# Performance work log

Hardware: AMD Instinct MI355X
Metric: run time of the kernel (lower is better)

The kernel has to match this reference:

```python
import jax, jax.numpy as jnp
import numpy as np

N = 100000   # nodes
E = 1600000  # edges
D = 64       # in_channels
H = 64       # hidden_channels
G = 1000     # number of graphs (100 nodes each)


def _xavier(key, fan_in, fan_out):
    a = np.sqrt(6.0 / (fan_in + fan_out)).astype(np.float32)
    return jax.random.uniform(key, (fan_in, fan_out), jnp.float32, -a, a)


def setup_inputs() -> dict:
    key = jax.random.key(0)
    ks = jax.random.split(key, 6)
    x = jax.random.normal(ks[0], (N, D), jnp.float32)
    edge_index = jax.random.randint(ks[1], (2, E), 0, N, dtype=jnp.int32)
    edge_weight = jax.random.uniform(ks[2], (E,), jnp.float32)
    # every graph id 0..G-1 occurs exactly N//G times (sorted)
    batch = (jnp.arange(N, dtype=jnp.int32) // (N // G)).astype(jnp.int32)
    W1 = _xavier(ks[3], D, H); b1 = jnp.zeros((H,), jnp.float32)
    W2 = _xavier(ks[4], H, H); b2 = jnp.zeros((H,), jnp.float32)
    W3 = _xavier(ks[5], H, 1); b3 = jnp.zeros((1,), jnp.float32)
    return dict(x=x, edge_index=edge_index, edge_weight=edge_weight, batch=batch,
                W1=W1, b1=b1, W2=W2, b2=b2, W3=W3, b3=b3)


def reference(x, edge_index, edge_weight, batch, W1, b1, W2, b2, W3, b3):
    src, dst = edge_index[0], edge_index[1]
    # nodes per graph (torch.bincount(batch)) and broadcast back to nodes
    counts = jax.ops.segment_sum(jnp.ones((N,), jnp.float32), batch, num_segments=G)
    cpn = counts[batch]  # [N]

    def mpnn_layer(h, W, b):
        # gather x_j, scale by edge weight, scatter-add to target nodes
        m = h[src] * edge_weight[:, None]              # [E, C]
        agg = jax.ops.segment_sum(m, dst, num_segments=N)  # [N, C]
        out = agg / cpn[:, None]                       # per-node normalize
        return out @ W + b

    h = jax.nn.sigmoid(mpnn_layer(x, W1, b1))
    h = jax.nn.sigmoid(mpnn_layer(h, W2, b2))
    h = mpnn_layer(h, W3, b3)                          # [N, 1]
    # global mean pool over each graph
    pooled = jax.ops.segment_sum(h, batch, num_segments=G) / counts[:, None]
    return pooled  # [G, 1]
```

## Files before the change

### kernel.cpp

```cpp
#include <hip/hip_runtime.h>
#include <hip/hip_fp16.h>
#include <math.h>

#define NN 100000
#define EE 1600000
#define GG 1000
#define NPG 100
#define NBUK 391
#define BCAP 4608
#define EPB 8192
#define NBINBLK ((EE + EPB - 1) / EPB)
#define GEMM1BLK ((NN + 127) / 128)
#define GEMM2BLK ((NN + 63) / 64)

typedef __attribute__((ext_vector_type(8))) short short8v;
typedef __attribute__((ext_vector_type(4))) float float4v;

__device__ __forceinline__ unsigned char f32_to_fp8(float a) {
    return (unsigned char)(__builtin_amdgcn_cvt_pk_fp8_f32(a, a, 0, false) & 0xFF);
}
__device__ __forceinline__ float fp8_to_f32(unsigned b) {
    return __builtin_amdgcn_cvt_f32_fp8((int)b, 0);
}
__device__ __forceinline__ unsigned short f32_to_bf16(float f) {
    unsigned u = __float_as_uint(f);
    unsigned r = u + 0x7FFFu + ((u >> 16) & 1u);
    return (unsigned short)(r >> 16);
}

#if __has_builtin(__builtin_amdgcn_cvt_pk_f32_fp8)
typedef float floatx2 __attribute__((ext_vector_type(2)));
#define HAVE_PK_CVT 1
#else
#define HAVE_PK_CVT 0
#endif

__device__ __forceinline__ void unpack4(unsigned dw, float* f) {
#if HAVE_PK_CVT
    floatx2 lo = __builtin_amdgcn_cvt_pk_f32_fp8(dw, false);
    floatx2 hi = __builtin_amdgcn_cvt_pk_f32_fp8(dw, true);
    f[0] = lo.x; f[1] = lo.y; f[2] = hi.x; f[3] = hi.y;
#else
    f[0] = fp8_to_f32(dw & 0xFF);
    f[1] = fp8_to_f32((dw >> 8) & 0xFF);
    f[2] = fp8_to_f32((dw >> 16) & 0xFF);
    f[3] = fp8_to_f32((dw >> 24) & 0xFF);
#endif
}

__device__ __forceinline__ float4v mfma16(short8v a, short8v b, float4v c) {
    return __builtin_amdgcn_mfma_f32_16x16x32_bf16(a, b, c, 0, 0, 0);
}
__device__ __forceinline__ short8v fp8x8_to_bf16frag(uint2 q) {
    float f[8];
    unpack4(q.x, f);
    unpack4(q.y, f + 4);
    short8v s;
#pragma unroll
    for (int j = 0; j < 8; j++) s[j] = (short)f32_to_bf16(f[j]);
    return s;
}
__device__ __forceinline__ short8v f32x8_to_bf16frag(float4 a, float4 b) {
    short8v s;
    s[0] = (short)f32_to_bf16(a.x); s[1] = (short)f32_to_bf16(a.y);
    s[2] = (short)f32_to_bf16(a.z); s[3] = (short)f32_to_bf16(a.w);
    s[4] = (short)f32_to_bf16(b.x); s[5] = (short)f32_to_bf16(b.y);
    s[6] = (short)f32_to_bf16(b.z); s[7] = (short)f32_to_bf16(b.w);
    return s;
}
template<int NT>
__device__ __forceinline__ void stageW(const float* __restrict__ W,
                                       unsigned short* Wt, int tid) {
    for (int i = tid; i < 4096; i += NT) {
        int k = i >> 6, c = i & 63;
        Wt[(c << 6) | (((k >> 3) ^ (c & 7)) << 3) | (k & 7)] = f32_to_bf16(W[i]);
    }
}
__device__ __forceinline__ short8v ldB(const unsigned short* Wt, int col, int g) {
    return *(const short8v*)&Wt[(col << 6) | ((g ^ (col & 7)) << 3)];
}
__device__ __forceinline__ void mfma_tile_store(short8v a_lo, short8v a_hi,
                                                const unsigned short* Wt,
                                                int row0, int lane,
                                                unsigned char* __restrict__ out, int n) {
    int rl = lane & 15, kg = lane >> 4;
#pragma unroll
    for (int ct = 0; ct < 4; ct++) {
        int col = ct * 16 + rl;
        short8v blo = ldB(Wt, col, kg);
        short8v bhi = ldB(Wt, col, 4 + kg);
        float4v acc = {0.f, 0.f, 0.f, 0.f};
        acc = mfma16(a_lo, blo, acc);
        acc = mfma16(a_hi, bhi, acc);
        int dr = (lane >> 4) * 4;
#pragma unroll
        for (int r = 0; r < 4; r++) {
            int R = row0 + dr + r;
            if (R < n) out[(size_t)R * 64 + col] = f32_to_fp8(acc[r]);
        }
    }
}

__global__ __launch_bounds__(512)
void k_binbound(const int* __restrict__ src, const int* __restrict__ dst,
                const float* __restrict__ ew, int* __restrict__ bukcnt,
                uint2* __restrict__ ep1, int* __restrict__ rowptr, int E) {
    __shared__ int hist[NBUK];
    __shared__ int gbase[NBUK];
    int tid = threadIdx.x;
    if (blockIdx.x == 0 && tid == 0) rowptr[NN] = EE;
    for (int i = tid; i < NBUK; i += 512) hist[i] = 0;
    __syncthreads();
    int base = blockIdx.x * EPB;
    int b[16], rank[16];
    unsigned x[16], w[16];
#pragma unroll
    for (int u = 0; u < 16; u++) {
        int e = base + u * 512 + tid;
        if (e < E) {
            int d = dst[e];
            b[u] = d >> 8;
            x[u] = ((unsigned)(d & 255) << 24) | (unsigned)src[e];
            w[u] = __float_as_uint(ew[e]);
            rank[u] = atomicAdd(&hist[b[u]], 1);
        } else b[u] = -1;
    }
    __syncthreads();
    for (int i = tid; i < NBUK; i += 512) {
        int h = hist[i];
        gbase[i] = h ? atomicAdd(&bukcnt[i], h) : 0;
    }
    __syncthreads();
#pragma unroll
    for (int u = 0; u < 16; u++) {
        if (b[u] >= 0) ep1[(size_t)b[u] * BCAP + gbase[b[u]] + rank[u]] = make_uint2(x[u], w[u]);
    }
}

__global__ __launch_bounds__(512)
void k_bin2gemm1(const uint2* __restrict__ ep1, const int* __restrict__ bukcnt,
                 unsigned* __restrict__ ep2, int* __restrict__ rowptr,
                 const float* __restrict__ x, const float* __restrict__ W1,
                 unsigned char* __restrict__ t, int n) {
    __shared__ __align__(16) unsigned char smem[41984];
    int tid = threadIdx.x;
    int bk = blockIdx.x;
    if (bk < NBUK) {
        uint2* stage = (uint2*)smem;
        int* h   = (int*)(smem + 36864);
        int* s   = h + 256;
        int* cur = s + 256;
        int* sc  = cur + 256;
        int v = (tid < NBUK) ? bukcnt[tid] : 0;
        sc[tid] = v;
        __syncthreads();
        for (int off = 1; off < 512; off <<= 1) {
            int tv = (tid >= off) ? sc[tid - off] : 0;
            __syncthreads();
            sc[tid] += tv;
            __syncthreads();
        }
        int cnt = bukcnt[bk];
        int base = sc[bk] - cnt;
        if (tid < 256) h[tid] = 0;
        __syncthreads();
        size_t ebase = (size_t)bk * BCAP;
        for (int e = tid; e < cnt; e += 512) {
            uint2 r = ep1[ebase + e];
            stage[e] = r;
            atomicAdd(&h[r.x >> 24], 1);
        }
        __syncthreads();
        if (tid < 256) s[tid] = h[tid];
        __syncthreads();
        for (int off = 1; off < 256; off <<= 1) {
            int tv = 0;
            if (tid < 256 && tid >= off) tv = s[tid - off];
            __syncthreads();
            if (tid < 256) s[tid] += tv;
            __syncthreads();
        }
        if (tid < 256) {
            int pfx = base + s[tid] - h[tid];
            int node = bk * 256 + tid;
            if (node < n) rowptr[node] = pfx;
            cur[tid] = pfx;
        }
        __syncthreads();
        for (int e = tid; e < cnt; e += 512) {
            uint2 r = stage[e];
            int pos = atomicAdd(&cur[r.x >> 24], 1);
            unsigned wq = (unsigned)fminf(__uint_as_float(r.y) * 32768.f + 0.5f, 32767.f);
            ep2[pos] = (wq << 17) | (r.x & 0x1FFFFu);
        }
    } else {
        unsigned short* Wt = (unsigned short*)smem;
        stageW<512>(W1, Wt, tid);
        __syncthreads();
        int w = tid >> 6, lane = tid & 63;
        int row0 = (bk - NBUK) * 128 + w * 16;
        int rl = lane & 15, kg = lane >> 4;
        int rsrc = row0 + rl;
        if (rsrc > n - 1) rsrc = n - 1;
        const float* ar = x + (size_t)rsrc * 64 + kg * 8;
        float4 f0 = *(const float4*)ar;
        float4 f1 = *(const float4*)(ar + 4);
        float4 f2 = *(const float4*)(ar + 32);
        float4 f3 = *(const float4*)(ar + 36);
        short8v a_lo = f32x8_to_bf16frag(f0, f1);
        short8v a_hi = f32x8_to_bf16frag(f2, f3);
        mfma_tile_store(a_lo, a_hi, Wt, row0, lane, t, n);
    }
}

__global__ __launch_bounds__(256)
void k_gemm64_mfma(const unsigned char* __restrict__ inp, const float* __restrict__ W,
                   unsigned char* __restrict__ out, int n) {
    __shared__ __align__(16) unsigned short Wt[64 * 64];
    int tid = threadIdx.x;
    stageW<256>(W, Wt, tid);
    __syncthreads();
    int w = tid >> 6, lane = tid & 63;
    int row0 = blockIdx.x * 64 + w * 16;
    int rl = lane & 15, kg = lane >> 4;
    int rsrc = row0 + rl;
    if (rsrc > n - 1) rsrc = n - 1;
    const unsigned char* ar = inp + (size_t)rsrc * 64 + kg * 8;
    uint2 qlo = *(const uint2*)ar;
    uint2 qhi = *(const uint2*)(ar + 32);
    short8v a_lo = fp8x8_to_bf16frag(qlo);
    short8v a_hi = fp8x8_to_bf16frag(qhi);
    mfma_tile_store(a_lo, a_hi, Wt, row0, lane, out, n);
}

template<int MODE>
__global__ __launch_bounds__(256)
void k_gather64(const unsigned char* __restrict__ t, const int* __restrict__ rowptr,
                const unsigned* __restrict__ ep, void* __restrict__ outp,
                const float* __restrict__ bv, const float* __restrict__ W3,
                int nq) {
    int wid = (blockIdx.x * blockDim.x + threadIdx.x) >> 6;
    int lane = threadIdx.x & 63;
    wid = __builtin_amdgcn_readfirstlane(wid);
    if (wid >= nq) return;
    int n0 = wid * 4;
    int q = lane >> 4;
    unsigned sl4 = (unsigned)(lane & 15) * 4u;

    int rp[5];
#pragma unroll
    for (int i = 0; i < 5; i++) rp[i] = rowptr[n0 + i];

    unsigned wl[4];
#pragma unroll
    for (int i = 0; i < 4; i++) {
        int e = rp[i] + lane;
        wl[i] = (e < rp[i + 1]) ? ep[e] : 0u;
    }

    unsigned vA[4][4];
#pragma unroll
    for (int i = 0; i < 4; i++) {
#pragma unroll
        for (int g = 0; g < 4; g++) {
            unsigned wq = __shfl(wl[i], g * 4 + q, 64);
            vA[i][g] = *(const unsigned*)(t + ((wq & 0x1FFFFu) * 64u + sl4));
        }
    }
    unsigned vB[4][4];
#pragma unroll
    for (int i = 0; i < 4; i++) {
        if (rp[i + 1] - rp[i] > 16) {
#pragma unroll
            for (int g = 0; g < 4; g++) {
                unsigned wq = __shfl(wl[i], 16 + g * 4 + q, 64);
                vB[i][g] = *(const unsigned*)(t + ((wq & 0x1FFFFu) * 64u + sl4));
            }
        }
    }

    const float Cn = 0x1p-15f / (float)NPG;
    float4 bb = ((const float4*)bv)[lane & 15];
    float4 w4 = (MODE == 1) ? ((const float4*)W3)[lane & 15] : make_float4(0, 0, 0, 0);

#pragma unroll
    for (int i = 0; i < 4; i++) {
        float ax = 0.f, ay = 0.f, az = 0.f, aw = 0.f;
#pragma unroll
        for (int g = 0; g < 4; g++) {
            unsigned wq = __shfl(wl[i], g * 4 + q, 64);
            float wt = (float)(wq >> 17);
            float f[4];
            unpack4(vA[i][g], f);
            ax = fmaf(wt, f[0], ax); ay = fmaf(wt, f[1], ay);
            az = fmaf(wt, f[2], az); aw = fmaf(wt, f[3], aw);
        }
        if (rp[i + 1] - rp[i] > 16) {
#pragma unroll
            for (int g = 0; g < 4; g++) {
                unsigned wq = __shfl(wl[i], 16 + g * 4 + q, 64);
                float wt = (float)(wq >> 17);
                float f[4];
                unpack4(vB[i][g], f);
                ax = fmaf(wt, f[0], ax); ay = fmaf(wt, f[1], ay);
                az = fmaf(wt, f[2], az); aw = fmaf(wt, f[3], aw);
            }
        }
        for (int e = rp[i] + 32 + q; e < rp[i + 1]; e += 4) {
            unsigned wq = ep[e];
            float wt = (float)(wq >> 17);
            float f[4];
            unpack4(*(const unsigned*)(t + ((wq & 0x1FFFFu) * 64u + sl4)), f);
            ax = fmaf(wt, f[0], ax); ay = fmaf(wt, f[1], ay);
            az = fmaf(wt, f[2], az); aw = fmaf(wt, f[3], aw);
        }
        ax += __shfl_xor(ax, 16, 64); ax += __shfl_xor(ax, 32, 64);
        ay += __shfl_xor(ay, 16, 64); ay += __shfl_xor(ay, 32, 64);
        az += __shfl_xor(az, 16, 64); az += __shfl_xor(az, 32, 64);
        aw += __shfl_xor(aw, 16, 64); aw += __shfl_xor(aw, 32, 64);
        float v0 = ax * Cn + bb.x, v1 = ay * Cn + bb.y;
        float v2 = az * Cn + bb.z, v3 = aw * Cn + bb.w;
        v0 = 1.f / (1.f + __expf(-v0));
        v1 = 1.f / (1.f + __expf(-v1));
        v2 = 1.f / (1.f + __expf(-v2));
        v3 = 1.f / (1.f + __expf(-v3));
        if (MODE == 0) {
            if (q == 0) {
                unsigned r = (unsigned)__builtin_amdgcn_cvt_pk_fp8_f32(v0, v1, 0, false);
                r = (unsigned)__builtin_amdgcn_cvt_pk_fp8_f32(v2, v3, (int)r, true);
                ((unsigned*)outp)[(size_t)(n0 + i) * 16 + (lane & 15)] = r;
            }
        } else {
            float d = v0 * w4.x + v1 * w4.y + v2 * w4.z + v3 * w4.w;
            d += __shfl_xor(d, 1, 64);
            d += __shfl_xor(d, 2, 64);
            d += __shfl_xor(d, 4, 64);
            d += __shfl_xor(d, 8, 64);
            if (lane == 0) ((float*)outp)[n0 + i] = d;
        }
    }
}

__global__ __launch_bounds__(256)
void k_y3pool(const float* __restrict__ y, const int* __restrict__ rowptr,
              const unsigned* __restrict__ ep,
              const float* __restrict__ b3, float* __restrict__ out) {
    __shared__ float red[256];
    int g = blockIdx.x;
    int tid = threadIdx.x;
    int ebeg = rowptr[g * NPG], eend = rowptr[g * NPG + NPG];
    float acc = 0.f;
    for (int e = ebeg + tid; e < eend; e += 256) {
        unsigned r = ep[e];
        unsigned off = (r & 0x1FFFFu) * 4u;
        acc = fmaf((float)(r >> 17), *(const float*)((const char*)y + off), acc);
    }
    red[tid] = acc;
    __syncthreads();
    for (int off = 128; off > 0; off >>= 1) {
        if (tid < off) red[tid] += red[tid + off];
        __syncthreads();
    }
    if (tid == 0) {
        out[g] = red[0] * 0x1p-15f / ((float)NPG * (float)NPG) + b3[0];
    }
}

extern "C" void kernel_launch(void* const* d_in, const int* in_sizes, int n_in,
                              void* d_out, int out_size, void* d_ws, size_t ws_size,
                              hipStream_t stream) {
    const float* x     = (const float*)d_in[0];
    const int*   ei    = (const int*)d_in[1];
    const int*   src   = ei;
    const int*   dst   = ei + EE;
    const float* ew    = (const float*)d_in[2];
    const float* W1    = (const float*)d_in[4];
    const float* b1    = (const float*)d_in[5];
    const float* W2    = (const float*)d_in[6];
    const float* b2    = (const float*)d_in[7];
    const float* W3    = (const float*)d_in[8];
    const float* b3    = (const float*)d_in[9];
    float* out = (float*)d_out;

    unsigned char* t   = (unsigned char*)d_ws;
    unsigned char* t2  = t + (size_t)NN * 64;
    unsigned char* hh8 = t2 + (size_t)NN * 64;
    float* y      = (float*)(hh8 + (size_t)NN * 64);
    unsigned* ep2 = (unsigned*)(y + NN);
    int*   bukcnt = (int*)(ep2 + EE);
    int*   rowptr = bukcnt + NBUK + 1;
    uint2* ep1    = (uint2*)(rowptr + NN + 2);

    hipMemsetAsync(bukcnt, 0, NBUK * sizeof(int), stream);

    k_binbound<<<NBINBLK, 512, 0, stream>>>(src, dst, ew, bukcnt, ep1, rowptr, EE);

    k_bin2gemm1<<<NBUK + GEMM1BLK, 512, 0, stream>>>(ep1, bukcnt, ep2, rowptr, x, W1, t, NN);

    int nq = NN / 4;
    int gblk = (nq * 64 + 255) / 256;

    k_gather64<0><<<gblk, 256, 0, stream>>>(t, rowptr, ep2, hh8, b1, nullptr, nq);

    k_gemm64_mfma<<<GEMM2BLK, 256, 0, stream>>>(hh8, W2, t2, NN);

    k_gather64<1><<<gblk, 256, 0, stream>>>(t2, rowptr, ep2, y, b2, W3, nq);

    k_y3pool<<<GG, 256, 0, stream>>>(y, rowptr, ep2, b3, out);
}
```

Before: 204.8 us.

## Make gather kernel persistent with software-prefetch of next quad's edge lists

```diff
diff --git a/kernel.cpp b/kernel.cpp
--- a/kernel.cpp
+++ b/kernel.cpp
@@ -12,6 +12,7 @@
 #define NBINBLK ((EE + EPB - 1) / EPB)
 #define GEMM1BLK ((NN + 127) / 128)
 #define GEMM2BLK ((NN + 63) / 64)
+#define GATHBLK 1536
 
 typedef __attribute__((ext_vector_type(8))) short short8v;
 typedef __attribute__((ext_vector_type(4))) float float4v;
@@ -239,105 +240,128 @@
                 const unsigned* __restrict__ ep, void* __restrict__ outp,
                 const float* __restrict__ bv, const float* __restrict__ W3,
                 int nq) {
-    int wid = (blockIdx.x * blockDim.x + threadIdx.x) >> 6;
     int lane = threadIdx.x & 63;
-    wid = __builtin_amdgcn_readfirstlane(wid);
-    if (wid >= nq) return;
-    int n0 = wid * 4;
+    int wv = (blockIdx.x * blockDim.x + threadIdx.x) >> 6;
+    wv = __builtin_amdgcn_readfirstlane(wv);
+    int nwv = (GATHBLK * 256) >> 6;
     int q = lane >> 4;
     unsigned sl4 = (unsigned)(lane & 15) * 4u;
-
-    int rp[5];
-#pragma unroll
-    for (int i = 0; i < 5; i++) rp[i] = rowptr[n0 + i];
-
-    unsigned wl[4];
-#pragma unroll
-    for (int i = 0; i < 4; i++) {
-        int e = rp[i] + lane;
-        wl[i] = (e < rp[i + 1]) ? ep[e] : 0u;
-    }
-
-    unsigned vA[4][4];
-#pragma unroll
-    for (int i = 0; i < 4; i++) {
-#pragma unroll
-        for (int g = 0; g < 4; g++) {
-            unsigned wq = __shfl(wl[i], g * 4 + q, 64);
-            vA[i][g] = *(const unsigned*)(t + ((wq & 0x1FFFFu) * 64u + sl4));
-        }
-    }
-    unsigned vB[4][4];
-#pragma unroll
-    for (int i = 0; i < 4; i++) {
-        if (rp[i + 1] - rp[i] > 16) {
-#pragma unroll
-            for (int g = 0; g < 4; g++) {
-                unsigned wq = __shfl(wl[i], 16 + g * 4 + q, 64);
-                vB[i][g] = *(const unsigned*)(t + ((wq & 0x1FFFFu) * 64u + sl4));
-            }
-        }
-    }
-
     const float Cn = 0x1p-15f / (float)NPG;
     float4 bb = ((const float4*)bv)[lane & 15];
     float4 w4 = (MODE == 1) ? ((const float4*)W3)[lane & 15] : make_float4(0, 0, 0, 0);
 
+    int quad = wv;
+    if (quad >= nq) return;
+
+    int rpA[5];
+    unsigned wlA[4];
+#pragma unroll
+    for (int i = 0; i < 5; i++) rpA[i] = rowptr[quad * 4 + i];
 #pragma unroll
     for (int i = 0; i < 4; i++) {
-        float ax = 0.f, ay = 0.f, az = 0.f, aw = 0.f;
-#pragma unroll
-        for (int g = 0; g < 4; g++) {
-            unsigned wq = __shfl(wl[i], g * 4 + q, 64);
-            float wt = (float)(wq >> 17);
-            float f[4];
-            unpack4(vA[i][g], f);
-            ax = fmaf(wt, f[0], ax); ay = fmaf(wt, f[1], ay);
-            az = fmaf(wt, f[2], az); aw = fmaf(wt, f[3], aw);
-        }
-        if (rp[i + 1] - rp[i] > 16) {
+        int e = rpA[i] + lane;
+        wlA[i] = (e < rpA[i + 1]) ? ep[e] : 0u;
+    }
+
+    while (true) {
+        int nxt = quad + nwv;
+        bool hn = nxt < nq;
+        int rpB[5];
+        if (hn) {
+#pragma unroll
+            for (int i = 0; i < 5; i++) rpB[i] = rowptr[nxt * 4 + i];
+        }
+        unsigned vA[4][4];
+#pragma unroll
+        for (int i = 0; i < 4; i++) {
 #pragma unroll
             for (int g = 0; g < 4; g++) {
-                unsigned wq = __shfl(wl[i], 16 + g * 4 + q, 64);
+                unsigned wq = __shfl(wlA[i], g * 4 + q, 64);
+                vA[i][g] = *(const unsigned*)(t + ((wq & 0x1FFFFu) * 64u + sl4));
+            }
+        }
+        unsigned vB[4][4];
+#pragma unroll
+        for (int i = 0; i < 4; i++) {
+            if (rpA[i + 1] - rpA[i] > 16) {
+#pragma unroll
+                for (int g = 0; g < 4; g++) {
+                    unsigned wq = __shfl(wlA[i], 16 + g * 4 + q, 64);
+                    vB[i][g] = *(const unsigned*)(t + ((wq & 0x1FFFFu) * 64u + sl4));
+                }
+            }
+        }
+        unsigned wlB[4];
+        if (hn) {
+#pragma unroll
+            for (int i = 0; i < 4; i++) {
+                int e = rpB[i] + lane;
+                wlB[i] = (e < rpB[i + 1]) ? ep[e] : 0u;
+            }
+        }
+        int n0 = quad * 4;
+#pragma unroll
+        for (int i = 0; i < 4; i++) {
+            float ax = 0.f, ay = 0.f, az = 0.f, aw = 0.f;
+#pragma unroll
+            for (int g = 0; g < 4; g++) {
+                unsigned wq = __shfl(wlA[i], g * 4 + q, 64);
                 float wt = (float)(wq >> 17);
                 float f[4];
-                unpack4(vB[i][g], f);
+                unpack4(vA[i][g], f);
                 ax = fmaf(wt, f[0], ax); ay = fmaf(wt, f[1], ay);
                 az = fmaf(wt, f[2], az); aw = fmaf(wt, f[3], aw);
             }
-        }
-        for (int e = rp[i] + 32 + q; e < rp[i + 1]; e += 4) {
-            unsigned wq = ep[e];
-            float wt = (float)(wq >> 17);
-            float f[4];
-            unpack4(*(const unsigned*)(t + ((wq & 0x1FFFFu) * 64u + sl4)), f);
-            ax = fmaf(wt, f[0], ax); ay = fmaf(wt, f[1], ay);
-            az = fmaf(wt, f[2], az); aw = fmaf(wt, f[3], aw);
-        }
-        ax += __shfl_xor(ax, 16, 64); ax += __shfl_xor(ax, 32, 64);
-        ay += __shfl_xor(ay, 16, 64); ay += __shfl_xor(ay, 32, 64);
-        az += __shfl_xor(az, 16, 64); az += __shfl_xor(az, 32, 64);
-        aw += __shfl_xor(aw, 16, 64); aw += __shfl_xor(aw, 32, 64);
-        float v0 = ax * Cn + bb.x, v1 = ay * Cn + bb.y;
-        float v2 = az * Cn + bb.z, v3 = aw * Cn + bb.w;
-        v0 = 1.f / (1.f + __expf(-v0));
-        v1 = 1.f / (1.f + __expf(-v1));
-        v2 = 1.f / (1.f + __expf(-v2));
-        v3 = 1.f / (1.f + __expf(-v3));
-        if (MODE == 0) {
-            if (q == 0) {
-                unsigned r = (unsigned)__builtin_amdgcn_cvt_pk_fp8_f32(v0, v1, 0, false);
-                r = (unsigned)__builtin_amdgcn_cvt_pk_fp8_f32(v2, v3, (int)r, true);
-                ((unsigned*)outp)[(size_t)(n0 + i) * 16 + (lane & 15)] = r;
-            }
-        } else {
-            float d = v0 * w4.x + v1 * w4.y + v2 * w4.z + v3 * w4.w;
-            d += __shfl_xor(d, 1, 64);
-            d += __shfl_xor(d, 2, 64);
-            d += __shfl_xor(d, 4, 64);
-            d += __shfl_xor(d, 8, 64);
-            if (lane == 0) ((float*)outp)[n0 + i] = d;
-        }
+            if (rpA[i + 1] - rpA[i] > 16) {
+#pragma unroll
+                for (int g = 0; g < 4; g++) {
+                    unsigned wq = __shfl(wlA[i], 16 + g * 4 + q, 64);
+                    float wt = (float)(wq >> 17);
+                    float f[4];
+                    unpack4(vB[i][g], f);
+                    ax = fmaf(wt, f[0], ax); ay = fmaf(wt, f[1], ay);
+                    az = fmaf(wt, f[2], az); aw = fmaf(wt, f[3], aw);
+                }
+            }
+            for (int e = rpA[i] + 32 + q; e < rpA[i + 1]; e += 4) {
+                unsigned wq = ep[e];
+                float wt = (float)(wq >> 17);
+                float f[4];
+                unpack4(*(const unsigned*)(t + ((wq & 0x1FFFFu) * 64u + sl4)), f);
+                ax = fmaf(wt, f[0], ax); ay = fmaf(wt, f[1], ay);
+                az = fmaf(wt, f[2], az); aw = fmaf(wt, f[3], aw);
+            }
+            ax += __shfl_xor(ax, 16, 64); ax += __shfl_xor(ax, 32, 64);
+            ay += __shfl_xor(ay, 16, 64); ay += __shfl_xor(ay, 32, 64);
+            az += __shfl_xor(az, 16, 64); az += __shfl_xor(az, 32, 64);
+            aw += __shfl_xor(aw, 16, 64); aw += __shfl_xor(aw, 32, 64);
+            float v0 = ax * Cn + bb.x, v1 = ay * Cn + bb.y;
+            float v2 = az * Cn + bb.z, v3 = aw * Cn + bb.w;
+            v0 = 1.f / (1.f + __expf(-v0));
+            v1 = 1.f / (1.f + __expf(-v1));
+            v2 = 1.f / (1.f + __expf(-v2));
+            v3 = 1.f / (1.f + __expf(-v3));
+            if (MODE == 0) {
+                if (q == 0) {
+                    unsigned r = (unsigned)__builtin_amdgcn_cvt_pk_fp8_f32(v0, v1, 0, false);
+                    r = (unsigned)__builtin_amdgcn_cvt_pk_fp8_f32(v2, v3, (int)r, true);
+                    ((unsigned*)outp)[(size_t)(n0 + i) * 16 + (lane & 15)] = r;
+                }
+            } else {
+                float d = v0 * w4.x + v1 * w4.y + v2 * w4.z + v3 * w4.w;
+                d += __shfl_xor(d, 1, 64);
+                d += __shfl_xor(d, 2, 64);
+                d += __shfl_xor(d, 4, 64);
+                d += __shfl_xor(d, 8, 64);
+                if (lane == 0) ((float*)outp)[n0 + i] = d;
+            }
+        }
+        if (!hn) break;
+        quad = nxt;
+#pragma unroll
+        for (int i = 0; i < 5; i++) rpA[i] = rpB[i];
+#pragma unroll
+        for (int i = 0; i < 4; i++) wlA[i] = wlB[i];
     }
 }
 
@@ -398,13 +422,12 @@
     k_bin2gemm1<<<NBUK + GEMM1BLK, 512, 0, stream>>>(ep1, bukcnt, ep2, rowptr, x, W1, t, NN);
 
     int nq = NN / 4;
-    int gblk = (nq * 64 + 255) / 256;
-
-    k_gather64<0><<<gblk, 256, 0, stream>>>(t, rowptr, ep2, hh8, b1, nullptr, nq);
+
+    k_gather64<0><<<GATHBLK, 256, 0, stream>>>(t, rowptr, ep2, hh8, b1, nullptr, nq);
 
     k_gemm64_mfma<<<GEMM2BLK, 256, 0, stream>>>(hh8, W2, t2, NN);
 
-    k_gather64<1><<<gblk, 256, 0, stream>>>(t2, rowptr, ep2, y, b2, W3, nq);
+    k_gather64<1><<<GATHBLK, 256, 0, stream>>>(t2, rowptr, ep2, y, b2, W3, nq);
 
     k_y3pool<<<GG, 256, 0, stream>>>(y, rowptr, ep2, b3, out);
 }
```

After: 213.2 us. 1.04x slower.

## Fuse layer-2 GEMM into first gather kernel via shared-memory MFMA tile

Applied to the files above, without the earlier changes.

```diff
diff --git a/kernel.cpp b/kernel.cpp
--- a/kernel.cpp
+++ b/kernel.cpp
@@ -11,7 +11,6 @@
 #define EPB 8192
 #define NBINBLK ((EE + EPB - 1) / EPB)
 #define GEMM1BLK ((NN + 127) / 128)
-#define GEMM2BLK ((NN + 63) / 64)
 
 typedef __attribute__((ext_vector_type(8))) short short8v;
 typedef __attribute__((ext_vector_type(4))) float float4v;
@@ -50,15 +49,6 @@
 
 __device__ __forceinline__ float4v mfma16(short8v a, short8v b, float4v c) {
     return __builtin_amdgcn_mfma_f32_16x16x32_bf16(a, b, c, 0, 0, 0);
-}
-__device__ __forceinline__ short8v fp8x8_to_bf16frag(uint2 q) {
-    float f[8];
-    unpack4(q.x, f);
-    unpack4(q.y, f + 4);
-    short8v s;
-#pragma unroll
-    for (int j = 0; j < 8; j++) s[j] = (short)f32_to_bf16(f[j]);
-    return s;
 }
 __device__ __forceinline__ short8v f32x8_to_bf16frag(float4 a, float4 b) {
     short8v s;
@@ -213,34 +203,20 @@
     }
 }
 
-__global__ __launch_bounds__(256)
-void k_gemm64_mfma(const unsigned char* __restrict__ inp, const float* __restrict__ W,
-                   unsigned char* __restrict__ out, int n) {
-    __shared__ __align__(16) unsigned short Wt[64 * 64];
-    int tid = threadIdx.x;
-    stageW<256>(W, Wt, tid);
-    __syncthreads();
-    int w = tid >> 6, lane = tid & 63;
-    int row0 = blockIdx.x * 64 + w * 16;
-    int rl = lane & 15, kg = lane >> 4;
-    int rsrc = row0 + rl;
-    if (rsrc > n - 1) rsrc = n - 1;
-    const unsigned char* ar = inp + (size_t)rsrc * 64 + kg * 8;
-    uint2 qlo = *(const uint2*)ar;
-    uint2 qhi = *(const uint2*)(ar + 32);
-    short8v a_lo = fp8x8_to_bf16frag(qlo);
-    short8v a_hi = fp8x8_to_bf16frag(qhi);
-    mfma_tile_store(a_lo, a_hi, Wt, row0, lane, out, n);
-}
-
 template<int MODE>
 __global__ __launch_bounds__(256)
 void k_gather64(const unsigned char* __restrict__ t, const int* __restrict__ rowptr,
                 const unsigned* __restrict__ ep, void* __restrict__ outp,
                 const float* __restrict__ bv, const float* __restrict__ W3,
+                const float* __restrict__ W2, unsigned char* __restrict__ t2,
                 int nq) {
-    int wid = (blockIdx.x * blockDim.x + threadIdx.x) >> 6;
-    int lane = threadIdx.x & 63;
+    __shared__ __align__(16) unsigned short Wt[4096];
+    __shared__ __align__(16) unsigned short H1[1024];
+    int tid = threadIdx.x;
+    if (MODE == 0) stageW<256>(W2, Wt, tid);
+
+    int wid = (blockIdx.x * blockDim.x + tid) >> 6;
+    int lane = tid & 63;
     wid = __builtin_amdgcn_readfirstlane(wid);
     if (wid >= nq) return;
     int n0 = wid * 4;
@@ -326,9 +302,15 @@
         v3 = 1.f / (1.f + __expf(-v3));
         if (MODE == 0) {
             if (q == 0) {
-                unsigned r = (unsigned)__builtin_amdgcn_cvt_pk_fp8_f32(v0, v1, 0, false);
-                r = (unsigned)__builtin_amdgcn_cvt_pk_fp8_f32(v2, v3, (int)r, true);
-                ((unsigned*)outp)[(size_t)(n0 + i) * 16 + (lane & 15)] = r;
+                int s = lane & 15;
+                int row = (tid >> 6) * 4 + i;
+                unsigned g = (unsigned)(s >> 1);
+                unsigned off = ((unsigned)row << 6) | ((g ^ (unsigned)(row & 7)) << 3)
+                             | ((unsigned)(s & 1) << 2);
+                H1[off    ] = f32_to_bf16(v0);
+                H1[off + 1] = f32_to_bf16(v1);
+                H1[off + 2] = f32_to_bf16(v2);
+                H1[off + 3] = f32_to_bf16(v3);
             }
         } else {
             float d = v0 * w4.x + v1 * w4.y + v2 * w4.z + v3 * w4.w;
@@ -337,6 +319,28 @@
             d += __shfl_xor(d, 4, 64);
             d += __shfl_xor(d, 8, 64);
             if (lane == 0) ((float*)outp)[n0 + i] = d;
+        }
+    }
+
+    if (MODE == 0) {
+        __syncthreads();
+        int w = tid >> 6;
+        int rl = lane & 15, kg = lane >> 4;
+        short8v a_lo = *(const short8v*)&H1[((unsigned)rl << 6)
+                        | (((unsigned)kg ^ (unsigned)(rl & 7)) << 3)];
+        short8v a_hi = *(const short8v*)&H1[((unsigned)rl << 6)
+                        | ((((unsigned)kg + 4u) ^ (unsigned)(rl & 7)) << 3)];
+        int col = w * 16 + rl;
+        short8v blo = ldB(Wt, col, kg);
+        short8v bhi = ldB(Wt, col, 4 + kg);
+        float4v acc = {0.f, 0.f, 0.f, 0.f};
+        acc = mfma16(a_lo, blo, acc);
+        acc = mfma16(a_hi, bhi, acc);
+        int row0 = blockIdx.x * 16;
+        int dr = kg * 4;
+#pragma unroll
+        for (int r = 0; r < 4; r++) {
+            t2[(size_t)(row0 + dr + r) * 64 + col] = f32_to_fp8(acc[r]);
         }
     }
 }
@@ -384,8 +388,7 @@
 
     unsigned char* t   = (unsigned char*)d_ws;
     unsigned char* t2  = t + (size_t)NN * 64;
-    unsigned char* hh8 = t2 + (size_t)NN * 64;
-    float* y      = (float*)(hh8 + (size_t)NN * 64);
+    float* y      = (float*)(t2 + (size_t)NN * 64);
     unsigned* ep2 = (unsigned*)(y + NN);
     int*   bukcnt = (int*)(ep2 + EE);
     int*   rowptr = bukcnt + NBUK + 1;
@@ -398,13 +401,11 @@
     k_bin2gemm1<<<NBUK + GEMM1BLK, 512, 0, stream>>>(ep1, bukcnt, ep2, rowptr, x, W1, t, NN);
 
     int nq = NN / 4;
-    int gblk = (nq * 64 + 255) / 256;
-
-    k_gather64<0><<<gblk, 256, 0, stream>>>(t, rowptr, ep2, hh8, b1, nullptr, nq);
-
-    k_gemm64_mfma<<<GEMM2BLK, 256, 0, stream>>>(hh8, W2, t2, NN);
-
-    k_gather64<1><<<gblk, 256, 0, stream>>>(t2, rowptr, ep2, y, b2, W3, nq);
+    int gblk = (nq * 64) / 256;
+
+    k_gather64<0><<<gblk, 256, 0, stream>>>(t, rowptr, ep2, nullptr, b1, nullptr, W2, t2, nq);
+
+    k_gather64<1><<<gblk, 256, 0, stream>>>(t2, rowptr, ep2, y, b2, W3, nullptr, nullptr, nq);
 
     k_y3pool<<<GG, 256, 0, stream>>>(y, rowptr, ep2, b3, out);
 }
```

After: 204.6 us. About the same (-0.1%).
